# Optimization experiments

Measured on AMD Instinct MI355X. Metric: run time of the kernel, lower is better.

## Reference

```python
import jax, jax.numpy as jnp
import numpy as np

N, P, K, H, W = 16, 2048, 512, 256, 256
ZTHRESH = 2.0          # PRUN_ZSCORE_THRESHOLD
MULT = 5               # HV_HYPOTHESIS_IN_MASK_MULTIPLIER


def setup_inputs() -> dict:
    key = jax.random.key(0)
    uv_img = jax.random.normal(key, (N, 2, H, W), dtype=jnp.float32)
    rng = np.random.default_rng(0)
    # mask points per instance (torch.where(mask[i]) made fixed-shape)
    pts = rng.integers(0, H, size=(N, P, 2)).astype(np.int32)
    # multinomial pair sampling without replacement: distinct indices per pair
    i0 = rng.integers(0, P, size=(N, K))
    off = rng.integers(1, P, size=(N, K))
    i1 = (i0 + off) % P
    pair_idx = np.stack([i0, i1], axis=-1).astype(np.int32)
    return {"uv_img": uv_img, "pts": jnp.asarray(pts), "pair_idx": jnp.asarray(pair_idx)}


def _gather_uv(uv_img, coords):
    # uv_img: [N,2,H,W], coords: [N,M,2] int -> [N,M,2] uv values
    n, _, h, w = uv_img.shape
    flat = coords[..., 0] * w + coords[..., 1]            # [N,M]
    uv_flat = uv_img.reshape(n, 2, h * w)                 # [N,2,HW]
    g = jnp.take_along_axis(uv_flat, flat[:, None, :], axis=2)  # [N,2,M]
    return jnp.transpose(g, (0, 2, 1))                    # [N,M,2]


def reference(uv_img, pts, pair_idx):
    # --- generate hypotheses (batched pinverse solver) ---
    p0 = jnp.take_along_axis(pts, pair_idx[..., 0:1], axis=1)  # [N,K,2]
    p1 = jnp.take_along_axis(pts, pair_idx[..., 1:2], axis=1)  # [N,K,2]
    uv0 = _gather_uv(uv_img, p0)                               # [N,K,2]
    uv1 = _gather_uv(uv_img, p1)                               # [N,K,2]
    A = jnp.stack((uv0, -uv1), axis=-1)                        # [N,K,2,2]
    Bv = (p1 - p0).astype(jnp.float32)[..., None]              # [N,K,2,1]  (-p0 + p1)
    X = jnp.matmul(jnp.linalg.pinv(A), Bv)                     # [N,K,2,1]
    x0 = X[:, :, 0, :]                                         # [N,K,1]
    Y = x0 * uv0 + p0.astype(jnp.float32)                      # [N,K,2] hypotheses

    # --- prune outliers (z-score, drop -> nan in torch; here masked) ---
    mean = jnp.mean(Y, axis=1, keepdims=True)
    std = jnp.std(Y, axis=1, keepdims=True, ddof=1)
    z = jnp.abs((Y - mean) / std)
    bad = jnp.any(z > ZTHRESH, axis=-1) | jnp.any(jnp.isnan(Y), axis=-1)  # [N,K]
    Yz = jnp.where(bad[..., None], 0.0, Y)                     # nan-hypotheses zeroed (as torch does)

    # --- hypothesis weights ---
    ptsf = pts.astype(jnp.float32)                             # [N,P,2]
    uv_p = _gather_uv(uv_img, pts)                             # [N,P,2]
    d = Y[:, :, None, :] - ptsf[:, None, :, :]                 # [N,K,P,2]
    a = d / jnp.linalg.norm(d, axis=-1, keepdims=True)
    b = jnp.einsum('nkpc,npc->nkp', a, uv_p) > 0               # direction agreement
    w = jnp.sum(b, axis=-1)                                    # [N,K] int
    match = Y.astype(jnp.int32)[:, :, None, :] == pts[:, None, :, :]
    h_in_mask = jnp.sum(match[..., 0] & match[..., 1], axis=-1)  # [N,K]
    factor = jnp.where(h_in_mask == 1, MULT, 1)
    w = (factor * w).astype(jnp.float32)
    w = jnp.where(bad, 0.0, w)                                 # outlier rows get 0 weight
    w = w / jnp.maximum(jnp.sum(w, axis=1, keepdims=True), 1.0)

    weighted_mean = jnp.sum(Yz * w[..., None], axis=1)         # [N,2]
    pixel_xy = weighted_mean[:, ::-1]                          # (row,col) -> (x,y)
    return pixel_xy
```

## Files before the change

kernel.cpp:

```cpp
#include <hip/hip_runtime.h>
#include <math.h>

#define N_ 16
#define P_ 2048
#define K_ 512
#define H_ 256
#define W_ 256
#define HW_ (H_ * W_)
#define ZT_ 2.0f

__global__ __launch_bounds__(512) void hough_main(
    const float* __restrict__ uv_img, const int* __restrict__ pts,
    const int* __restrict__ pair, float4* __restrict__ partial) {
  int b = blockIdx.x;
  int n = b >> 4, kt = b & 15;
  int tid = threadIdx.x;
  int lane = tid & 63, wave = tid >> 6;

  __shared__ float2 Ys[K_];
  __shared__ float4 sf[256];
  __shared__ int2 si[256];
  __shared__ unsigned char badf[K_];
  __shared__ float red[8][3];
  __shared__ float bc[4];

  const int2* pts2 = (const int2*)pts + n * P_;
  const float* base = uv_img + (size_t)n * 2 * HW_;

  {
    int2 pr = ((const int2*)pair)[n * K_ + tid];
    int2 p0 = pts2[pr.x];
    int2 p1 = pts2[pr.y];
    float u00 = base[p0.x * W_ + p0.y];
    float u01 = base[HW_ + p0.x * W_ + p0.y];
    float u10 = base[p1.x * W_ + p1.y];
    float u11 = base[HW_ + p1.x * W_ + p1.y];
    float B0 = (float)(p1.x - p0.x);
    float B1 = (float)(p1.y - p0.y);
    float det = u10 * u01 - u00 * u11;
    float x0 = (u10 * B1 - B0 * u11) / det;
    Ys[tid] = make_float2(x0 * u00 + (float)p0.x, x0 * u01 + (float)p0.y);
  }
  __syncthreads();

  float2 y = Ys[tid];
  float a0 = y.x, a1 = y.y;
  for (int off = 32; off >= 1; off >>= 1) {
    a0 += __shfl_down(a0, off);
    a1 += __shfl_down(a1, off);
  }
  if (lane == 0) { red[wave][0] = a0; red[wave][1] = a1; }
  __syncthreads();
  if (tid == 0) {
    float t0 = 0.f, t1 = 0.f;
    for (int i = 0; i < 8; i++) { t0 += red[i][0]; t1 += red[i][1]; }
    bc[0] = t0 / (float)K_;
    bc[1] = t1 / (float)K_;
  }
  __syncthreads();
  float m0 = bc[0], m1 = bc[1];
  float e0 = y.x - m0, e1 = y.y - m1;
  a0 = e0 * e0;
  a1 = e1 * e1;
  for (int off = 32; off >= 1; off >>= 1) {
    a0 += __shfl_down(a0, off);
    a1 += __shfl_down(a1, off);
  }
  if (lane == 0) { red[wave][0] = a0; red[wave][1] = a1; }
  __syncthreads();
  if (tid == 0) {
    float t0 = 0.f, t1 = 0.f;
    for (int i = 0; i < 8; i++) { t0 += red[i][0]; t1 += red[i][1]; }
    bc[2] = sqrtf(t0 / (float)(K_ - 1));
    bc[3] = sqrtf(t1 / (float)(K_ - 1));
  }
  __syncthreads();
  float sd0 = bc[2], sd1 = bc[3];
  int bd = (fabsf(e0 / sd0) > ZT_) | (fabsf(e1 / sd1) > ZT_) |
           (y.x != y.x) | (y.y != y.y);
  badf[tid] = (unsigned char)bd;

  int k = kt * 32 + (tid >> 4);
  int pl = tid & 15;
  float2 yk = Ys[k];
  int iy0 = (int)yk.x, iy1 = (int)yk.y;
  int cnt = 0, hm = 0;

  for (int t = 0; t < 8; t++) {
    __syncthreads();
    int pp = tid & 255, ch = tid >> 8;
    int p = t * 256 + pp;
    int2 pc = pts2[p];
    float g = base[ch * HW_ + pc.x * W_ + pc.y];
    ((float*)&sf[pp])[2 + ch] = g;
    if (ch == 0) {
      ((float*)&sf[pp])[0] = (float)pc.x;
      ((float*)&sf[pp])[1] = (float)pc.y;
      si[pp] = pc;
    }
    __syncthreads();
#pragma unroll 4
    for (int i = 0; i < 16; i++) {
      int idx = pl + 16 * i;
      float4 f = sf[idx];
      int2 ii = si[idx];
      float d0 = yk.x - f.x;
      float d1 = yk.y - f.y;
      float dot = d0 * f.z + d1 * f.w;
      cnt += (dot > 0.f) ? 1 : 0;
      hm += ((iy0 == ii.x) & (iy1 == ii.y)) ? 1 : 0;
    }
  }

  for (int off = 8; off >= 1; off >>= 1) {
    cnt += __shfl_down(cnt, off);
    hm += __shfl_down(hm, off);
  }
  float w = 0.f, s0 = 0.f, s1 = 0.f;
  if (pl == 0) {
    if (badf[k]) {
      w = 0.f;
    } else {
      w = (float)cnt * ((hm == 1) ? 5.0f : 1.0f);
      s0 = w * yk.x;
      s1 = w * yk.y;
    }
  }
  for (int off = 32; off >= 1; off >>= 1) {
    w += __shfl_down(w, off);
    s0 += __shfl_down(s0, off);
    s1 += __shfl_down(s1, off);
  }
  __syncthreads();
  if (lane == 0) { red[wave][0] = w; red[wave][1] = s0; red[wave][2] = s1; }
  __syncthreads();
  if (tid == 0) {
    float tw = 0.f, t0 = 0.f, t1 = 0.f;
    for (int i = 0; i < 8; i++) {
      tw += red[i][0];
      t0 += red[i][1];
      t1 += red[i][2];
    }
    partial[b] = make_float4(tw, t0, t1, 0.f);
  }
}

__global__ __launch_bounds__(256) void hough_final(
    const float4* __restrict__ partial, float* __restrict__ out) {
  int tid = threadIdx.x;
  float4 p = partial[tid];
  float sw = p.x, s0 = p.y, s1 = p.z;
  for (int off = 8; off >= 1; off >>= 1) {
    sw += __shfl_down(sw, off);
    s0 += __shfl_down(s0, off);
    s1 += __shfl_down(s1, off);
  }
  if ((tid & 15) == 0) {
    int n = tid >> 4;
    float den = fmaxf(sw, 1.0f);
    out[n * 2 + 0] = s1 / den;
    out[n * 2 + 1] = s0 / den;
  }
}

extern "C" void kernel_launch(void* const* d_in, const int* in_sizes, int n_in,
                              void* d_out, int out_size, void* d_ws,
                              size_t ws_size, hipStream_t stream) {
  const float* uv_img = (const float*)d_in[0];
  const int* pts = (const int*)d_in[1];
  const int* pair = (const int*)d_in[2];
  float* out = (float*)d_out;
  float4* partial = (float4*)d_ws;

  hipLaunchKernelGGL(hough_main, dim3(256), dim3(512), 0, stream, uv_img, pts,
                     pair, partial);
  hipLaunchKernelGGL(hough_final, dim3(1), dim3(256), 0, stream, partial, out);
}
```

Measured before the change: 28.73 us.

## Split into precompute and vote kernels with full-P shared tile and fused final reduction

Moves the per-point uv gather and the per-instance hypothesis generation and z-score pruning into a precompute kernel, so they are no longer redone in each of the 16 blocks per instance. The vote kernel then loads all 2048 points into shared memory at once, with a precomputed dot-product constant and packed coordinates. This cuts the inner loop to one fma pair plus an integer compare, and removes the per-tile barriers. The final reduction moves into the vote kernel through a last-block atomic counter. The cost is workspace round-trips through global memory and 32KB of shared memory per block, which may limit occupancy.

```diff
diff --git a/kernel.cpp b/kernel.cpp
--- a/kernel.cpp
+++ b/kernel.cpp
@@ -8,27 +8,34 @@
 #define W_ 256
 #define HW_ (H_ * W_)
 #define ZT_ 2.0f
-
-__global__ __launch_bounds__(512) void hough_main(
+#define GBLK_ 128
+#define KB_ 32
+#define KPB_ 16
+
+__global__ __launch_bounds__(256) void k_pre(
     const float* __restrict__ uv_img, const int* __restrict__ pts,
-    const int* __restrict__ pair, float4* __restrict__ partial) {
-  int b = blockIdx.x;
-  int n = b >> 4, kt = b & 15;
+    const int* __restrict__ pair, float2* __restrict__ uvp,
+    float2* __restrict__ Yg, int* __restrict__ bad, int* __restrict__ done) {
   int tid = threadIdx.x;
-  int lane = tid & 63, wave = tid >> 6;
-
-  __shared__ float2 Ys[K_];
-  __shared__ float4 sf[256];
-  __shared__ int2 si[256];
-  __shared__ unsigned char badf[K_];
-  __shared__ float red[8][3];
-  __shared__ float bc[4];
-
+  if (blockIdx.x < GBLK_) {
+    int id = blockIdx.x * 256 + tid;
+    int2 c = ((const int2*)pts)[id];
+    const float* base = uv_img + (size_t)(id >> 11) * 2 * HW_;
+    int o = c.x * W_ + c.y;
+    uvp[id] = make_float2(base[o], base[HW_ + o]);
+    return;
+  }
+  int n = blockIdx.x - GBLK_;
+  if (tid == 0) done[n] = 0;
   const int2* pts2 = (const int2*)pts + n * P_;
+  const int2* pr2 = (const int2*)pair + n * K_;
   const float* base = uv_img + (size_t)n * 2 * HW_;
 
-  {
-    int2 pr = ((const int2*)pair)[n * K_ + tid];
+  float2 ya, yb;
+#pragma unroll
+  for (int h = 0; h < 2; h++) {
+    int k = tid + h * 256;
+    int2 pr = pr2[k];
     int2 p0 = pts2[pr.x];
     int2 p1 = pts2[pr.y];
     float u00 = base[p0.x * W_ + p0.y];
@@ -39,12 +46,15 @@
     float B1 = (float)(p1.y - p0.y);
     float det = u10 * u01 - u00 * u11;
     float x0 = (u10 * B1 - B0 * u11) / det;
-    Ys[tid] = make_float2(x0 * u00 + (float)p0.x, x0 * u01 + (float)p0.y);
-  }
-  __syncthreads();
-
-  float2 y = Ys[tid];
-  float a0 = y.x, a1 = y.y;
+    float2 y = make_float2(x0 * u00 + (float)p0.x, x0 * u01 + (float)p0.y);
+    if (h == 0) ya = y; else yb = y;
+    Yg[n * K_ + k] = y;
+  }
+
+  __shared__ float red[4][2];
+  __shared__ float bc[4];
+  int wave = tid >> 6, lane = tid & 63;
+  float a0 = ya.x + yb.x, a1 = ya.y + yb.y;
   for (int off = 32; off >= 1; off >>= 1) {
     a0 += __shfl_down(a0, off);
     a1 += __shfl_down(a1, off);
@@ -52,16 +62,17 @@
   if (lane == 0) { red[wave][0] = a0; red[wave][1] = a1; }
   __syncthreads();
   if (tid == 0) {
-    float t0 = 0.f, t1 = 0.f;
-    for (int i = 0; i < 8; i++) { t0 += red[i][0]; t1 += red[i][1]; }
+    float t0 = red[0][0] + red[1][0] + red[2][0] + red[3][0];
+    float t1 = red[0][1] + red[1][1] + red[2][1] + red[3][1];
     bc[0] = t0 / (float)K_;
     bc[1] = t1 / (float)K_;
   }
   __syncthreads();
   float m0 = bc[0], m1 = bc[1];
-  float e0 = y.x - m0, e1 = y.y - m1;
-  a0 = e0 * e0;
-  a1 = e1 * e1;
+  float ea0 = ya.x - m0, ea1 = ya.y - m1;
+  float eb0 = yb.x - m0, eb1 = yb.y - m1;
+  a0 = ea0 * ea0 + eb0 * eb0;
+  a1 = ea1 * ea1 + eb1 * eb1;
   for (int off = 32; off >= 1; off >>= 1) {
     a0 += __shfl_down(a0, off);
     a1 += __shfl_down(a1, off);
@@ -69,97 +80,109 @@
   if (lane == 0) { red[wave][0] = a0; red[wave][1] = a1; }
   __syncthreads();
   if (tid == 0) {
-    float t0 = 0.f, t1 = 0.f;
-    for (int i = 0; i < 8; i++) { t0 += red[i][0]; t1 += red[i][1]; }
+    float t0 = red[0][0] + red[1][0] + red[2][0] + red[3][0];
+    float t1 = red[0][1] + red[1][1] + red[2][1] + red[3][1];
     bc[2] = sqrtf(t0 / (float)(K_ - 1));
     bc[3] = sqrtf(t1 / (float)(K_ - 1));
   }
   __syncthreads();
   float sd0 = bc[2], sd1 = bc[3];
-  int bd = (fabsf(e0 / sd0) > ZT_) | (fabsf(e1 / sd1) > ZT_) |
-           (y.x != y.x) | (y.y != y.y);
-  badf[tid] = (unsigned char)bd;
-
-  int k = kt * 32 + (tid >> 4);
+  int bda = (fabsf(ea0 / sd0) > ZT_) | (fabsf(ea1 / sd1) > ZT_) |
+            (ya.x != ya.x) | (ya.y != ya.y);
+  int bdb = (fabsf(eb0 / sd0) > ZT_) | (fabsf(eb1 / sd1) > ZT_) |
+            (yb.x != yb.x) | (yb.y != yb.y);
+  bad[n * K_ + tid] = bda;
+  bad[n * K_ + tid + 256] = bdb;
+}
+
+__global__ __launch_bounds__(256) void k_vote(
+    const int* __restrict__ pts, const float2* __restrict__ uvp,
+    const float2* __restrict__ Yg, const int* __restrict__ bad,
+    float* __restrict__ pw, float* __restrict__ ps0, float* __restrict__ ps1,
+    int* __restrict__ done, float* __restrict__ out) {
+  int b = blockIdx.x, tid = threadIdx.x;
+  int n = b >> 5, kt = b & (KB_ - 1);
+  __shared__ float4 sf[P_];
+  __shared__ float red[4][3];
+  __shared__ int sflag;
+  const int2* pts2 = (const int2*)pts + n * P_;
+  const float2* uvn = uvp + n * P_;
+
+#pragma unroll
+  for (int j = 0; j < 8; j++) {
+    int p = j * 256 + tid;
+    int2 pc = pts2[p];
+    float2 uc = uvn[p];
+    float c = (float)pc.x * uc.x + (float)pc.y * uc.y;
+    int pk = (pc.x << 8) | pc.y;
+    sf[p] = make_float4(uc.x, uc.y, c, __int_as_float(pk));
+  }
+
+  int k = kt * KPB_ + (tid >> 4);
   int pl = tid & 15;
-  float2 yk = Ys[k];
+  float2 yk = Yg[n * K_ + k];
   int iy0 = (int)yk.x, iy1 = (int)yk.y;
+  int mk = (((unsigned)iy0 < 256u) & ((unsigned)iy1 < 256u))
+               ? ((iy0 << 8) | iy1) : -1;
+  __syncthreads();
+
   int cnt = 0, hm = 0;
-
-  for (int t = 0; t < 8; t++) {
-    __syncthreads();
-    int pp = tid & 255, ch = tid >> 8;
-    int p = t * 256 + pp;
-    int2 pc = pts2[p];
-    float g = base[ch * HW_ + pc.x * W_ + pc.y];
-    ((float*)&sf[pp])[2 + ch] = g;
-    if (ch == 0) {
-      ((float*)&sf[pp])[0] = (float)pc.x;
-      ((float*)&sf[pp])[1] = (float)pc.y;
-      si[pp] = pc;
-    }
-    __syncthreads();
-#pragma unroll 4
-    for (int i = 0; i < 16; i++) {
-      int idx = pl + 16 * i;
-      float4 f = sf[idx];
-      int2 ii = si[idx];
-      float d0 = yk.x - f.x;
-      float d1 = yk.y - f.y;
-      float dot = d0 * f.z + d1 * f.w;
-      cnt += (dot > 0.f) ? 1 : 0;
-      hm += ((iy0 == ii.x) & (iy1 == ii.y)) ? 1 : 0;
-    }
+#pragma unroll 8
+  for (int i = 0; i < P_ / 16; i++) {
+    float4 f = sf[pl + (i << 4)];
+    float dot = fmaf(yk.x, f.x, fmaf(yk.y, f.y, -f.z));
+    cnt += (dot > 0.f) ? 1 : 0;
+    hm += (__float_as_int(f.w) == mk) ? 1 : 0;
   }
 
   for (int off = 8; off >= 1; off >>= 1) {
-    cnt += __shfl_down(cnt, off);
-    hm += __shfl_down(hm, off);
+    cnt += __shfl_down(cnt, off, 16);
+    hm += __shfl_down(hm, off, 16);
   }
   float w = 0.f, s0 = 0.f, s1 = 0.f;
-  if (pl == 0) {
-    if (badf[k]) {
-      w = 0.f;
-    } else {
-      w = (float)cnt * ((hm == 1) ? 5.0f : 1.0f);
-      s0 = w * yk.x;
-      s1 = w * yk.y;
-    }
+  if (pl == 0 && !bad[n * K_ + k]) {
+    w = (float)cnt * ((hm == 1) ? 5.0f : 1.0f);
+    s0 = w * yk.x;
+    s1 = w * yk.y;
   }
   for (int off = 32; off >= 1; off >>= 1) {
     w += __shfl_down(w, off);
     s0 += __shfl_down(s0, off);
     s1 += __shfl_down(s1, off);
   }
-  __syncthreads();
+  int wave = tid >> 6, lane = tid & 63;
   if (lane == 0) { red[wave][0] = w; red[wave][1] = s0; red[wave][2] = s1; }
   __syncthreads();
   if (tid == 0) {
-    float tw = 0.f, t0 = 0.f, t1 = 0.f;
-    for (int i = 0; i < 8; i++) {
-      tw += red[i][0];
-      t0 += red[i][1];
-      t1 += red[i][2];
+    float tw = red[0][0] + red[1][0] + red[2][0] + red[3][0];
+    float t0 = red[0][1] + red[1][1] + red[2][1] + red[3][1];
+    float t1 = red[0][2] + red[1][2] + red[2][2] + red[3][2];
+    pw[b] = tw;
+    ps0[b] = t0;
+    ps1[b] = t1;
+    int old = __hip_atomic_fetch_add(&done[n], 1, __ATOMIC_ACQ_REL,
+                                     __HIP_MEMORY_SCOPE_AGENT);
+    sflag = (old == KB_ - 1);
+  }
+  __syncthreads();
+  if (sflag && tid < KB_) {
+    int i = (n << 5) + tid;
+    float fw = __hip_atomic_load(&pw[i], __ATOMIC_RELAXED,
+                                 __HIP_MEMORY_SCOPE_AGENT);
+    float f0 = __hip_atomic_load(&ps0[i], __ATOMIC_RELAXED,
+                                 __HIP_MEMORY_SCOPE_AGENT);
+    float f1 = __hip_atomic_load(&ps1[i], __ATOMIC_RELAXED,
+                                 __HIP_MEMORY_SCOPE_AGENT);
+    for (int off = 16; off >= 1; off >>= 1) {
+      fw += __shfl_down(fw, off, 32);
+      f0 += __shfl_down(f0, off, 32);
+      f1 += __shfl_down(f1, off, 32);
     }
-    partial[b] = make_float4(tw, t0, t1, 0.f);
-  }
-}
-
-__global__ __launch_bounds__(256) void hough_final(
-    const float4* __restrict__ partial, float* __restrict__ out) {
-  int tid = threadIdx.x;
-  float4 p = partial[tid];
-  float sw = p.x, s0 = p.y, s1 = p.z;
-  for (int off = 8; off >= 1; off >>= 1) {
-    sw += __shfl_down(sw, off);
-    s0 += __shfl_down(s0, off);
-    s1 += __shfl_down(s1, off);
-  }
-  if ((tid & 15) == 0) {
-    int n = tid >> 4;
-    float den = fmaxf(sw, 1.0f);
-    out[n * 2 + 0] = s1 / den;
-    out[n * 2 + 1] = s0 / den;
+    if (tid == 0) {
+      float den = fmaxf(fw, 1.0f);
+      out[n * 2 + 0] = f1 / den;
+      out[n * 2 + 1] = f0 / den;
+    }
   }
 }
 
@@ -170,9 +193,17 @@
   const int* pts = (const int*)d_in[1];
   const int* pair = (const int*)d_in[2];
   float* out = (float*)d_out;
-  float4* partial = (float4*)d_ws;
-
-  hipLaunchKernelGGL(hough_main, dim3(256), dim3(512), 0, stream, uv_img, pts,
-                     pair, partial);
-  hipLaunchKernelGGL(hough_final, dim3(1), dim3(256), 0, stream, partial, out);
+
+  float2* uvp = (float2*)d_ws;
+  float2* Yg = uvp + N_ * P_;
+  int* bad = (int*)(Yg + N_ * K_);
+  float* pw = (float*)(bad + N_ * K_);
+  float* ps0 = pw + N_ * KB_;
+  float* ps1 = ps0 + N_ * KB_;
+  int* done = (int*)(ps1 + N_ * KB_);
+
+  hipLaunchKernelGGL(k_pre, dim3(GBLK_ + N_), dim3(256), 0, stream, uv_img,
+                     pts, pair, uvp, Yg, bad, done);
+  hipLaunchKernelGGL(k_vote, dim3(N_ * KB_), dim3(256), 0, stream, pts, uvp,
+                     Yg, bad, pw, ps0, ps1, done, out);
 }
```

After: 26.46 us. 1.09x faster.
